# Optimization experiments

Hardware: AMD Instinct MI355X
Metric: run time of the kernel (lower is better)

## Reference

```python
import jax, jax.numpy as jnp
import numpy as np

NEG = -1e30  # finite stand-in for -inf to keep logsumexp NaN-free


def setup_inputs() -> dict:
    key = jax.random.key(0)
    k1, k2 = jax.random.split(key)
    B, T, C, L = 1024, 256, 128, 48
    # ctc_batch_cost expects softmax probabilities over C classes (blank = C-1)
    y_pred = jax.nn.softmax(jax.random.normal(k1, (B, T, C), dtype=jnp.float32), axis=-1)
    labels = jax.random.randint(k2, (B, L), 0, C - 1, dtype=jnp.int32)  # values in [0, C-2]
    return {"y_pred": y_pred, "labels": labels}


def _lse3(a, b, c):
    m = jnp.maximum(jnp.maximum(a, b), c)
    return m + jnp.log(jnp.exp(a - m) + jnp.exp(b - m) + jnp.exp(c - m))


def reference(y_pred, labels):
    """CTC loss matching keras.backend.ctc_batch_cost (blank = num_classes-1),
    with full input_length=T and label_length=L as in CTCLayer.call.
    Returns per-example loss of shape [B, 1]."""
    eps = 1e-7  # keras.backend.epsilon()
    logp = jnp.log(y_pred + eps)              # [B, T, C]
    B, T, C = y_pred.shape
    L = labels.shape[1]
    S = 2 * L + 1                             # extended label length (blanks interleaved)
    blank = C - 1

    # extended label: blank, l1, blank, l2, ..., lL, blank  -> [B, S]
    ext = jnp.full((B, S), blank, dtype=labels.dtype).at[:, 1::2].set(labels)
    # transition s-2 -> s allowed iff ext[s] != blank and ext[s] != ext[s-2]
    can_skip = jnp.concatenate(
        [jnp.zeros((B, 2), dtype=bool), (ext[:, 2:] != blank) & (ext[:, 2:] != ext[:, :-2])],
        axis=1)                               # [B, S]

    # log-probs gathered at extended-label symbols: [T, B, S]
    lpe = jnp.take_along_axis(jnp.transpose(logp, (1, 0, 2)),
                              jnp.broadcast_to(ext[None], (T, B, S)), axis=2)

    alpha0 = (jnp.full((B, S), NEG, dtype=logp.dtype)
              .at[:, 0].set(lpe[0, :, 0])
              .at[:, 1].set(lpe[0, :, 1]))

    pad1 = jnp.full((B, 1), NEG, dtype=logp.dtype)
    pad2 = jnp.full((B, 2), NEG, dtype=logp.dtype)

    def step(alpha, lp_t):
        a2 = jnp.concatenate([pad1, alpha[:, :-1]], axis=1)
        a3 = jnp.where(can_skip, jnp.concatenate([pad2, alpha[:, :-2]], axis=1), NEG)
        alpha = _lse3(alpha, a2, a3) + lp_t
        return alpha, None

    alphaT, _ = jax.lax.scan(step, alpha0, lpe[1:])
    loss = -jnp.logaddexp(alphaT[:, S - 1], alphaT[:, S - 2])  # end at last blank or last label
    return loss[:, None]                       # [B, 1], matching ctc_batch_cost
```

## Files before the change

### kernel.cpp

```cpp
#include <hip/hip_runtime.h>


#define TT 256
#define CC 128
#define LL 48
#define BS 16
#define NB (TT / BS)

template<int CTRL>
__device__ __forceinline__ float dpp_mv(float x) {
    union { float f; int i; } u, r;
    u.f = x;
    r.i = __builtin_amdgcn_update_dpp(0, u.i, CTRL, 0xF, 0xF, false);
    return r.f;
}
__device__ __forceinline__ float rdlane(float x, int l) {
    union { float f; int i; } u, r;
    u.f = x;
    r.i = __builtin_amdgcn_readlane(u.i, l);
    return r.f;
}

__global__ __launch_bounds__(256) void ctc_fwd_v8(
    const float* __restrict__ y,
    const int* __restrict__ labels,
    float* __restrict__ out)
{
    const int lane = threadIdx.x & 63;
    const int wave = threadIdx.x >> 6;
    const int b = blockIdx.x * 4 + wave;
    const float EPS = 1e-7f;

    int lab = CC - 1;
    if (lane < LL) lab = labels[b * LL + lane];
    const int labprev = __shfl_up(lab, 1);
    const float csf = ((lane > 0) && (lane < LL) && (lab != labprev)) ? 1.0f : 0.0f;

    const float* p = y + (size_t)b * TT * CC + lab;

    float A[BS], B[BS], C[BS], D[BS];
    float a0 = (lane == 0) ? 1.0f : 0.0f;
    float a1 = 0.0f;
    int lg = 0;

#define ISSUE(buf, bi_) do {                                              \
    const int _t0 = (bi_) * BS;                                           \
    _Pragma("unroll")                                                     \
    for (int _j = 0; _j < BS; ++_j) {                                     \
        int _t = _t0 + _j; _t = (_t < TT) ? _t : (TT - 1);     \
        (buf)[_j] = p[(size_t)_t * CC];                                   \
    } } while (0)

#define PIN(buf) do {                                                     \
    _Pragma("unroll")                                                     \
    for (int _j = 0; _j < BS; ++_j)                                       \
        asm volatile("" : "+v"((buf)[_j]));   \
    } while (0)

#define STEP(pv) do {                                                     \
    const float _pl = (pv) + EPS;                                         \
    const float _pb = rdlane((pv), 63) + EPS;    \
    const float _pp = dpp_mv<0x138>(a1);         \
    const float _a0o = a0;                                                \
    a0 = (_a0o + _pp) * _pb;                                              \
    a1 = (a1 + _a0o + csf * _pp) * _pl;                                   \
    } while (0)

#define RESCALE do {                                                      \
    float _m = fmaxf(a0, a1);                                             \
    _m = fmaxf(_m, dpp_mv<0x111>(_m));                     \
    _m = fmaxf(_m, dpp_mv<0x112>(_m));                     \
    _m = fmaxf(_m, dpp_mv<0x114>(_m));                     \
    _m = fmaxf(_m, dpp_mv<0x118>(_m));                     \
    _m = fmaxf(_m, dpp_mv<0x142>(_m));                  \
    _m = fmaxf(_m, dpp_mv<0x143>(_m));        \
    const float _mm = rdlane(_m, 63);                                     \
    int _e; (void)frexpf(_mm, &_e);                                       \
    a0 = ldexpf(a0, -_e);                                                 \
    a1 = ldexpf(a1, -_e);                                                 \
    lg += _e;                                                             \
    } while (0)

#define BODY(cons, dst, bi_) do {                                         \
    ISSUE(dst, (bi_) + 3);             \
    PIN(cons);                                                            \
    _Pragma("unroll")                                                     \
    for (int _k = 0; _k < BS; ++_k) {                                     \
        STEP((cons)[_k]);                                                 \
        if ((_k & 7) == 7) RESCALE;                                       \
    } } while (0)

    ISSUE(A, 0);
    ISSUE(B, 1);
    ISSUE(C, 2);
    for (int i = 0; i < NB; i += 4) {
        BODY(A, D, i);
        BODY(B, A, i + 1);
        BODY(C, B, i + 2);
        BODY(D, C, i + 3);
    }

    const float v95 = rdlane(a1, 47);
    const float v96 = rdlane(a0, 48);
    if (lane == 0) {
        const float s = fmaxf(v95 + v96, 1e-37f);
        out[b] = -(__logf(s) + (float)lg * 0.69314718056f);
    }

#undef ISSUE
#undef PIN
#undef STEP
#undef RESCALE
#undef BODY
}

extern "C" void kernel_launch(void* const* d_in, const int* in_sizes, int n_in,
                              void* d_out, int out_size, void* d_ws, size_t ws_size,
                              hipStream_t stream) {
    const float* y = (const float*)d_in[0];
    const int* labels = (const int*)d_in[1];
    float* out = (float*)d_out;
    const int B = in_sizes[0] / (TT * CC);
    ctc_fwd_v8<<<B / 4, 256, 0, stream>>>(y, labels, out);
}
```

Before: 29.48 us.

## Load full probability rows coalesced and gather label columns via ds_bpermute

Each lane now loads a contiguous float2 of the 128-class row per timestep, giving fully coalesced row loads, instead of a scattered per-label gather. The label-column values are then redistributed across lanes with two ds_bpermute operations and a select, and the blank comes from lane 63's high element. The gather for a block of timesteps is separated from the serial recurrence, and the outer loop is fully unrolled with prefetch skipped past the end. This cuts the number of memory transactions but adds LDS-crossbar permute work and more register pressure on the critical path.

```diff
diff --git a/kernel.cpp b/kernel.cpp
--- a/kernel.cpp
+++ b/kernel.cpp
@@ -6,6 +6,8 @@
 #define LL 48
 #define BS 16
 #define NB (TT / BS)
+
+typedef float f32x2 __attribute__((ext_vector_type(2)));
 
 template<int CTRL>
 __device__ __forceinline__ float dpp_mv(float x) {
@@ -21,7 +23,7 @@
     return r.f;
 }
 
-__global__ __launch_bounds__(256) void ctc_fwd_v8(
+__global__ __launch_bounds__(256) void ctc_fwd_v9(
     const float* __restrict__ y,
     const int* __restrict__ labels,
     float* __restrict__ out)
@@ -35,21 +37,21 @@
     if (lane < LL) lab = labels[b * LL + lane];
     const int labprev = __shfl_up(lab, 1);
     const float csf = ((lane > 0) && (lane < LL) && (lab != labprev)) ? 1.0f : 0.0f;
+    const int  bidx = (lab >> 1) << 2;
+    const bool odd  = (lab & 1);
 
-    const float* p = y + (size_t)b * TT * CC + lab;
+    const f32x2* p2 = (const f32x2*)(y + (size_t)b * TT * CC) + lane;
 
-    float A[BS], B[BS], C[BS], D[BS];
+    f32x2 A[BS], B[BS], C[BS], D[BS];
     float a0 = (lane == 0) ? 1.0f : 0.0f;
     float a1 = 0.0f;
     int lg = 0;
 
 #define ISSUE(buf, bi_) do {                                              \
-    const int _t0 = (bi_) * BS;                                           \
     _Pragma("unroll")                                                     \
-    for (int _j = 0; _j < BS; ++_j) {                                     \
-        int _t = _t0 + _j; _t = (_t < TT) ? _t : (TT - 1);     \
-        (buf)[_j] = p[(size_t)_t * CC];                                   \
-    } } while (0)
+    for (int _j = 0; _j < BS; ++_j)                                       \
+        (buf)[_j] = p2[(size_t)((bi_) * BS + _j) * (CC / 2)];             \
+    } while (0)
 
 #define PIN(buf) do {                                                     \
     _Pragma("unroll")                                                     \
@@ -57,13 +59,11 @@
         asm volatile("" : "+v"((buf)[_j]));   \
     } while (0)
 
-#define STEP(pv) do {                                                     \
-    const float _pl = (pv) + EPS;                                         \
-    const float _pb = rdlane((pv), 63) + EPS;    \
+#define STEP2(plv, pbv) do {                                              \
     const float _pp = dpp_mv<0x138>(a1);         \
     const float _a0o = a0;                                                \
-    a0 = (_a0o + _pp) * _pb;                                              \
-    a1 = (a1 + _a0o + csf * _pp) * _pl;                                   \
+    a0 = (_a0o + _pp) * (pbv);                                            \
+    a1 = (a1 + _a0o + csf * _pp) * (plv);                                 \
     } while (0)
 
 #define RESCALE do {                                                      \
@@ -82,23 +82,29 @@
     } while (0)
 
 #define BODY(cons, dst, bi_) do {                                         \
-    ISSUE(dst, (bi_) + 3);             \
+    if ((bi_) + 3 < NB) ISSUE(dst, (bi_) + 3);                            \
     PIN(cons);                                                            \
+    float _pl[BS], _pb[BS];                                               \
     _Pragma("unroll")                                                     \
     for (int _k = 0; _k < BS; ++_k) {                                     \
-        STEP((cons)[_k]);                                                 \
+        const int _lo = __builtin_amdgcn_ds_bpermute(bidx, __float_as_int((cons)[_k].x)); \
+        const int _hi = __builtin_amdgcn_ds_bpermute(bidx, __float_as_int((cons)[_k].y)); \
+        _pl[_k] = __int_as_float(odd ? _hi : _lo) + EPS;                  \
+        _pb[_k] = rdlane((cons)[_k].y, 63) + EPS;          \
+    }                                                                     \
+    _Pragma("unroll")                                                     \
+    for (int _k = 0; _k < BS; ++_k) {                                     \
+        STEP2(_pl[_k], _pb[_k]);                                          \
         if ((_k & 7) == 7) RESCALE;                                       \
     } } while (0)
 
     ISSUE(A, 0);
     ISSUE(B, 1);
     ISSUE(C, 2);
-    for (int i = 0; i < NB; i += 4) {
-        BODY(A, D, i);
-        BODY(B, A, i + 1);
-        BODY(C, B, i + 2);
-        BODY(D, C, i + 3);
-    }
+    BODY(A, D, 0);  BODY(B, A, 1);  BODY(C, B, 2);  BODY(D, C, 3);
+    BODY(A, D, 4);  BODY(B, A, 5);  BODY(C, B, 6);  BODY(D, C, 7);
+    BODY(A, D, 8);  BODY(B, A, 9);  BODY(C, B, 10); BODY(D, C, 11);
+    BODY(A, D, 12); BODY(B, A, 13); BODY(C, B, 14); BODY(D, C, 15);
 
     const float v95 = rdlane(a1, 47);
     const float v96 = rdlane(a0, 48);
@@ -109,7 +115,7 @@
 
 #undef ISSUE
 #undef PIN
-#undef STEP
+#undef STEP2
 #undef RESCALE
 #undef BODY
 }
@@ -121,5 +127,5 @@
     const int* labels = (const int*)d_in[1];
     float* out = (float*)d_out;
     const int B = in_sizes[0] / (TT * CC);
-    ctc_fwd_v8<<<B / 4, 256, 0, stream>>>(y, labels, out);
+    ctc_fwd_v9<<<B / 4, 256, 0, stream>>>(y, labels, out);
 }
```

Measured after the change: 28.13 us. -4.6%, faster.
